# Performance work log

Hardware: AMD Instinct MI355X
Metric: run time of the kernel (lower is better)

Reference implementation:

```python
import jax, jax.numpy as jnp
import numpy as np

B, K, H, W = 64, 128, 64, 64
N_BOXES = 256
ALPHA, BETA = 1.0, 0.5


def setup_inputs() -> dict:
    key = jax.random.key(0)
    k1, k2, k3, k4, k5, k6 = jax.random.split(key, 6)
    cams = jax.random.normal(k1, (B, K, H, W), dtype=jnp.float32)
    concepts_gt = (jax.random.uniform(k2, (B, K)) < 0.3).astype(jnp.float32)
    box_b = jax.random.randint(k3, (N_BOXES,), 0, B)
    box_c = jax.random.randint(k4, (N_BOXES,), 0, K)
    ys = jnp.sort(jax.random.randint(k5, (N_BOXES, 2), 0, H), axis=1)
    xs = jnp.sort(jax.random.randint(k6, (N_BOXES, 2), 0, W), axis=1)
    y0, y1 = ys[:, 0], jnp.maximum(ys[:, 1], ys[:, 0] + 1)
    x0, x1 = xs[:, 0], jnp.maximum(xs[:, 1], xs[:, 0] + 1)
    return {"cams": cams, "concepts_gt": concepts_gt,
            "box_b": box_b, "box_c": box_c,
            "y0": y0, "y1": y1, "x0": x0, "x1": x1}


def _bce_with_logits(z, y):
    # stable: -(y*log_sigmoid(z) + (1-y)*log_sigmoid(-z))
    return -(y * jax.nn.log_sigmoid(z) + (1.0 - y) * jax.nn.log_sigmoid(-z))


def reference(cams, concepts_gt, box_b, box_c, y0, y1, x0, x1):
    h, w = cams.shape[2], cams.shape[3]
    # 1) global classification loss: max-pool over HxW -> BCE -> mean
    logits = jnp.max(cams, axis=(2, 3))                       # (B, K)
    cls_loss = _bce_with_logits(logits, concepts_gt).mean()
    # 2) per-box localization loss (fully vectorized over boxes)
    cam_box = cams[box_b, box_c]                              # (N, H, W)
    s = jax.nn.sigmoid(cam_box)
    rows = jnp.arange(h)[None, :, None]                       # (1, H, 1)
    cols = jnp.arange(w)[None, None, :]                       # (1, 1, W)
    mask = ((rows >= y0[:, None, None]) & (rows < y1[:, None, None]) &
            (cols >= x0[:, None, None]) & (cols < x1[:, None, None])
            ).astype(cams.dtype)                              # (N, H, W)
    eps = 1e-6
    inside = (((s - 1.0) ** 2) * mask).sum((1, 2)) / (mask.sum((1, 2)) + eps)
    outside = ((s ** 2) * (1.0 - mask)).sum((1, 2)) / ((1.0 - mask).sum((1, 2)) + eps)
    loc_loss = (inside + outside).mean()                      # sum / num_boxes
    return ALPHA * cls_loss + BETA * loc_loss
```

## Files before the change

kernel.cpp:

```cpp
#include <hip/hip_runtime.h>
#include <math.h>

#define BB   64
#define KK   128
#define HH   64
#define WW   64
#define HW   (HH*WW)
#define NBOX 256
#define NCLS (BB*KK)

__global__ __launch_bounds__(256) void main_kernel(
    const float* __restrict__ cams,
    const float* __restrict__ gt,
    const int* __restrict__ box_b, const int* __restrict__ box_c,
    const int* __restrict__ by0, const int* __restrict__ by1,
    const int* __restrict__ bx0, const int* __restrict__ bx1,
    float* __restrict__ ws)
{
    const int blk = blockIdx.x;
    const int t   = threadIdx.x;
    __shared__ float red[8];

    if (blk < NCLS) {
        const float4* p = (const float4*)(cams + (size_t)blk * HW);
        float m = -INFINITY;
        #pragma unroll
        for (int j = 0; j < 4; ++j) {
            float4 v = p[t + 256 * j];
            m = fmaxf(m, fmaxf(fmaxf(v.x, v.y), fmaxf(v.z, v.w)));
        }
        #pragma unroll
        for (int off = 32; off >= 1; off >>= 1)
            m = fmaxf(m, __shfl_down(m, off, 64));
        const int wave = t >> 6;
        if ((t & 63) == 0) red[wave] = m;
        __syncthreads();
        if (t == 0) {
            float z = fmaxf(fmaxf(red[0], red[1]), fmaxf(red[2], red[3]));
            float y = gt[blk];
            ws[blk] = fmaxf(z, 0.f) - z * y + log1pf(expf(-fabsf(z)));
        }
    } else {
        const int n  = blk - NCLS;
        const int b  = box_b[n];
        const int c  = box_c[n];
        const int y0 = by0[n], y1 = by1[n];
        const int x0 = bx0[n], x1 = bx1[n];
        const float4* p = (const float4*)(cams + ((size_t)b * KK + c) * HW);

        float ins = 0.f, outs = 0.f;
        #pragma unroll
        for (int j = 0; j < 4; ++j) {
            const int i4  = t + 256 * j;
            float4 v = p[i4];
            const int pix = i4 * 4;
            const int row = pix >> 6;
            const int col = pix & 63;
            const bool rin = (row >= y0) && (row < y1);
            float vv[4] = {v.x, v.y, v.z, v.w};
            #pragma unroll
            for (int e = 0; e < 4; ++e) {
                float s = 1.f / (1.f + expf(-vv[e]));
                const int cc = col + e;
                const bool in = rin && (cc >= x0) && (cc < x1);
                float d = s - 1.f;
                if (in) ins  += d * d;
                else    outs += s * s;
            }
        }
        #pragma unroll
        for (int off = 32; off >= 1; off >>= 1) {
            ins  += __shfl_down(ins,  off, 64);
            outs += __shfl_down(outs, off, 64);
        }
        const int wave = t >> 6;
        if ((t & 63) == 0) { red[wave] = ins; red[4 + wave] = outs; }
        __syncthreads();
        if (t == 0) {
            float I = red[0] + red[1] + red[2] + red[3];
            float O = red[4] + red[5] + red[6] + red[7];
            float area = (float)((y1 - y0) * (x1 - x0));
            ws[NCLS + n] = I / (area + 1e-6f) + O / ((float)HW - area + 1e-6f);
        }
    }
}

__global__ __launch_bounds__(256) void reduce_kernel(
    const float* __restrict__ ws, float* __restrict__ out)
{
    const int t = threadIdx.x;
    __shared__ float red[8];

    float sc = 0.f;
    #pragma unroll
    for (int j = 0; j < NCLS / 256; ++j) sc += ws[t + 256 * j];
    float sb = ws[NCLS + t];

    #pragma unroll
    for (int off = 32; off >= 1; off >>= 1) {
        sc += __shfl_down(sc, off, 64);
        sb += __shfl_down(sb, off, 64);
    }
    const int wave = t >> 6;
    if ((t & 63) == 0) { red[wave] = sc; red[4 + wave] = sb; }
    __syncthreads();
    if (t == 0) {
        float cls = red[0] + red[1] + red[2] + red[3];
        float box = red[4] + red[5] + red[6] + red[7];
        out[0] = 1.0f * cls / (float)NCLS + 0.5f * box / (float)NBOX;
    }
}

extern "C" void kernel_launch(void* const* d_in, const int* in_sizes, int n_in,
                              void* d_out, int out_size, void* d_ws, size_t ws_size,
                              hipStream_t stream) {
    const float* cams = (const float*)d_in[0];
    const float* gt   = (const float*)d_in[1];
    const int*   bb   = (const int*)d_in[2];
    const int*   bc   = (const int*)d_in[3];
    const int*   y0   = (const int*)d_in[4];
    const int*   y1   = (const int*)d_in[5];
    const int*   x0   = (const int*)d_in[6];
    const int*   x1   = (const int*)d_in[7];
    float* ws  = (float*)d_ws;
    float* out = (float*)d_out;

    main_kernel<<<NCLS + NBOX, 256, 0, stream>>>(cams, gt, bb, bc, y0, y1, x0, x1, ws);
    reduce_kernel<<<1, 256, 0, stream>>>(ws, out);
}
```

Before: 201.2 us.

## Assign one wavefront per CAM map instead of one block

Each (b,k) max-pool and each box loss is now handled by a single 64-lane wavefront rather than a 256-thread block, which removes the LDS cross-wave reduction and __syncthreads. Each lane issues 8 float4 loads per batch before computing, raising memory-level parallelism per thread. Row and column indices are rederived for the new lane-to-pixel mapping. The trade-off is fewer threads per map and higher register use for the load buffers, which may lower occupancy.

```diff
diff --git a/kernel.cpp b/kernel.cpp
--- a/kernel.cpp
+++ b/kernel.cpp
@@ -8,6 +8,7 @@
 #define HW   (HH*WW)
 #define NBOX 256
 #define NCLS (BB*KK)
+#define NWAVE (NCLS + NBOX)
 
 __global__ __launch_bounds__(256) void main_kernel(
     const float* __restrict__ cams,
@@ -17,70 +18,74 @@
     const int* __restrict__ bx0, const int* __restrict__ bx1,
     float* __restrict__ ws)
 {
-    const int blk = blockIdx.x;
-    const int t   = threadIdx.x;
-    __shared__ float red[8];
+    const int gw   = (blockIdx.x * 256 + threadIdx.x) >> 6;
+    const int lane = threadIdx.x & 63;
+    if (gw >= NWAVE) return;
 
-    if (blk < NCLS) {
-        const float4* p = (const float4*)(cams + (size_t)blk * HW);
+    if (gw < NCLS) {
+        const float4* p = (const float4*)(cams + (size_t)gw * HW);
         float m = -INFINITY;
+        float4 v[8];
         #pragma unroll
-        for (int j = 0; j < 4; ++j) {
-            float4 v = p[t + 256 * j];
-            m = fmaxf(m, fmaxf(fmaxf(v.x, v.y), fmaxf(v.z, v.w)));
-        }
+        for (int j = 0; j < 8; ++j) v[j] = p[lane + 64 * j];
+        #pragma unroll
+        for (int j = 0; j < 8; ++j)
+            m = fmaxf(m, fmaxf(fmaxf(v[j].x, v[j].y), fmaxf(v[j].z, v[j].w)));
+        #pragma unroll
+        for (int j = 0; j < 8; ++j) v[j] = p[lane + 64 * (8 + j)];
+        #pragma unroll
+        for (int j = 0; j < 8; ++j)
+            m = fmaxf(m, fmaxf(fmaxf(v[j].x, v[j].y), fmaxf(v[j].z, v[j].w)));
+
         #pragma unroll
         for (int off = 32; off >= 1; off >>= 1)
             m = fmaxf(m, __shfl_down(m, off, 64));
-        const int wave = t >> 6;
-        if ((t & 63) == 0) red[wave] = m;
-        __syncthreads();
-        if (t == 0) {
-            float z = fmaxf(fmaxf(red[0], red[1]), fmaxf(red[2], red[3]));
-            float y = gt[blk];
-            ws[blk] = fmaxf(z, 0.f) - z * y + log1pf(expf(-fabsf(z)));
+
+        if (lane == 0) {
+            float z = m;
+            float y = gt[gw];
+            ws[gw] = fmaxf(z, 0.f) - z * y + log1pf(expf(-fabsf(z)));
         }
     } else {
-        const int n  = blk - NCLS;
+        const int n  = gw - NCLS;
         const int b  = box_b[n];
         const int c  = box_c[n];
         const int y0 = by0[n], y1 = by1[n];
         const int x0 = bx0[n], x1 = bx1[n];
         const float4* p = (const float4*)(cams + ((size_t)b * KK + c) * HW);
 
+        const int col0 = (4 * lane) & 63;
         float ins = 0.f, outs = 0.f;
         #pragma unroll
-        for (int j = 0; j < 4; ++j) {
-            const int i4  = t + 256 * j;
-            float4 v = p[i4];
-            const int pix = i4 * 4;
-            const int row = pix >> 6;
-            const int col = pix & 63;
-            const bool rin = (row >= y0) && (row < y1);
-            float vv[4] = {v.x, v.y, v.z, v.w};
+        for (int batch = 0; batch < 2; ++batch) {
+            float4 v[8];
             #pragma unroll
-            for (int e = 0; e < 4; ++e) {
-                float s = 1.f / (1.f + expf(-vv[e]));
-                const int cc = col + e;
-                const bool in = rin && (cc >= x0) && (cc < x1);
-                float d = s - 1.f;
-                if (in) ins  += d * d;
-                else    outs += s * s;
+            for (int j = 0; j < 8; ++j) v[j] = p[lane + 64 * (8 * batch + j)];
+            #pragma unroll
+            for (int j = 0; j < 8; ++j) {
+                const int row = (lane >> 4) + 4 * (8 * batch + j);
+                const bool rin = (row >= y0) && (row < y1);
+                float vv[4] = {v[j].x, v[j].y, v[j].z, v[j].w};
+                #pragma unroll
+                for (int e = 0; e < 4; ++e) {
+                    float s = 1.f / (1.f + expf(-vv[e]));
+                    const int cc = col0 + e;
+                    const bool in = rin && (cc >= x0) && (cc < x1);
+                    float d = s - 1.f;
+                    if (in) ins  += d * d;
+                    else    outs += s * s;
+                }
             }
         }
+
         #pragma unroll
         for (int off = 32; off >= 1; off >>= 1) {
             ins  += __shfl_down(ins,  off, 64);
             outs += __shfl_down(outs, off, 64);
         }
-        const int wave = t >> 6;
-        if ((t & 63) == 0) { red[wave] = ins; red[4 + wave] = outs; }
-        __syncthreads();
-        if (t == 0) {
-            float I = red[0] + red[1] + red[2] + red[3];
-            float O = red[4] + red[5] + red[6] + red[7];
+        if (lane == 0) {
             float area = (float)((y1 - y0) * (x1 - x0));
-            ws[NCLS + n] = I / (area + 1e-6f) + O / ((float)HW - area + 1e-6f);
+            ws[gw] = ins / (area + 1e-6f) + outs / ((float)HW - area + 1e-6f);
         }
     }
 }
@@ -125,6 +130,7 @@
     float* ws  = (float*)d_ws;
     float* out = (float*)d_out;
 
-    main_kernel<<<NCLS + NBOX, 256, 0, stream>>>(cams, gt, bb, bc, y0, y1, x0, x1, ws);
+    const int nblocks = (NWAVE * 64 + 255) / 256;
+    main_kernel<<<nblocks, 256, 0, stream>>>(cams, gt, bb, bc, y0, y1, x0, x1, ws);
     reduce_kernel<<<1, 256, 0, stream>>>(ws, out);
 }
```

Measured after the change: 203.1 us. Within noise of the previous version (+0.9%).
